# Performance work log

Hardware: AMD Instinct MI355X
Metric: run time of the kernel (lower is better)

The kernel has to match this reference:

```python
import jax, jax.numpy as jnp
import numpy as np

B, L, D, H, T = 64, 512, 768, 384, 9  # batch, seq_len, hidden, hidden//2, num_tags


def setup_inputs() -> dict:
    key = jax.random.key(0)
    ks = jax.random.split(key, 8)
    return {
        "encoder_out": jax.random.normal(ks[0], (B, L, D), jnp.float32),
        "ner_labels": jax.random.randint(ks[1], (B, L), 0, T),
        "mask": jnp.ones((B, L), jnp.bool_),
        "W1": jax.random.normal(ks[2], (D, H), jnp.float32) / np.sqrt(D).astype(np.float32),
        "b1": jnp.zeros((H,), jnp.float32),
        "W2": jax.random.normal(ks[3], (H, T), jnp.float32) / np.sqrt(H).astype(np.float32),
        "b2": jnp.zeros((T,), jnp.float32),
        "start_trans": jax.random.uniform(ks[4], (T,), jnp.float32, -0.1, 0.1),
        "end_trans": jax.random.uniform(ks[5], (T,), jnp.float32, -0.1, 0.1),
        "trans": jax.random.uniform(ks[6], (T, T), jnp.float32, -0.1, 0.1),
    }


def _crf_nll(emissions, tags, mask, start_trans, end_trans, trans):
    """-mean log-likelihood, matching pytorch-crf forward (reduction='mean')."""
    maskf = mask.astype(emissions.dtype)
    # ---- numerator: score of the gold tag path ----
    emit = jnp.take_along_axis(emissions, tags[..., None], axis=-1)[..., 0]  # [B,L]
    emit_score = jnp.sum(emit * maskf, axis=1)
    tr = trans[tags[:, :-1], tags[:, 1:]]  # [B,L-1]
    tr_score = jnp.sum(tr * maskf[:, 1:], axis=1)
    last_idx = jnp.sum(mask.astype(jnp.int32), axis=1) - 1
    last_tags = jnp.take_along_axis(tags, last_idx[:, None], axis=1)[:, 0]
    numer = start_trans[tags[:, 0]] + emit_score + tr_score + end_trans[last_tags]
    # ---- denominator: forward algorithm (log partition) via scan ----
    alpha0 = start_trans[None, :] + emissions[:, 0]          # [B,T]
    em_rest = jnp.swapaxes(emissions[:, 1:], 0, 1)           # [L-1,B,T]
    mk_rest = jnp.swapaxes(maskf[:, 1:], 0, 1)               # [L-1,B]

    def step(alpha, xs):
        e_t, m_t = xs
        nxt = jax.nn.logsumexp(alpha[:, :, None] + trans[None, :, :] + e_t[:, None, :], axis=1)
        return jnp.where(m_t[:, None] > 0, nxt, alpha), None

    alpha, _ = jax.lax.scan(step, alpha0, (em_rest, mk_rest))
    denom = jax.nn.logsumexp(alpha + end_trans[None, :], axis=1)
    return -jnp.mean(numer - denom)


def reference(encoder_out, ner_labels, mask, W1, b1, W2, b2, start_trans, end_trans, trans):
    # proj: Linear -> GELU (exact erf, torch default) -> Dropout (identity in eval)
    h = jax.nn.gelu(encoder_out @ W1 + b1, approximate=False)
    emissions = h @ W2 + b2  # [B,L,T]
    return _crf_nll(emissions, ner_labels, mask, start_trans, end_trans, trans)
```

## Files before the change

### kernel.cpp

```cpp
#include <hip/hip_runtime.h>
#include <hip/hip_bf16.h>
#include <math.h>

#define B_ 64
#define L_ 512
#define D_ 768
#define H_ 384
#define T_ 9
#define M_ (B_ * L_)

typedef __attribute__((ext_vector_type(8))) short short8;
typedef __attribute__((ext_vector_type(4))) float f32x4;

__device__ __forceinline__ unsigned short f2bf(float f) {
    unsigned u = __float_as_uint(f);
    u += 0x7FFFu + ((u >> 16) & 1u);
    return (unsigned short)(u >> 16);
}

__device__ __forceinline__ unsigned pkbf2(float a, float b) {
    __hip_bfloat162 h = __float22bfloat162_rn(float2{a, b});
    return *(unsigned*)&h;
}

__device__ __forceinline__ float gelu_fast(float x) {
    float z2 = 1.5957691216f * x + 0.0713548162726f * x * x * x;
    return x / (1.f + __expf(-z2));
}

__device__ __forceinline__ float wredf(float v) {
#pragma unroll
    for (int m = 32; m >= 1; m >>= 1) v += __shfl_xor(v, m, 64);
    return v;
}

__device__ __forceinline__ void sync_lds() {
    asm volatile("s_waitcnt lgkmcnt(0)\n\ts_barrier" ::: "memory");
}

__global__ __launch_bounds__(256) void prep_kernel(
    const float* __restrict__ W1, const float* __restrict__ W2,
    unsigned short* __restrict__ W1F, unsigned short* __restrict__ W2F,
    float* __restrict__ out)
{
    if (blockIdx.x == 0 && threadIdx.x == 0) out[0] = 0.f;
    const int g    = blockIdx.x * 4 + (threadIdx.x >> 6);
    const int lane = threadIdx.x & 63;
    const int lm   = lane & 15;
    const int q    = lane >> 4;
    if (g < 576) {
        const int nt = g / 24;
        const int kc = g - nt * 24;
        const int n  = nt * 16 + lm;
        short8 v;
#pragma unroll
        for (int j = 0; j < 8; ++j)
            v[j] = (short)f2bf(W1[(size_t)(kc * 32 + q * 8 + j) * H_ + n]);
        *(short8*)(W1F + ((size_t)g * 64 + lane) * 8) = v;
    } else if (g < 588) {
        const int kk = g - 576;
        short8 v;
#pragma unroll
        for (int j = 0; j < 8; ++j) {
            int k = kk * 32 + q * 8 + j;
            v[j] = (lm < 9) ? (short)f2bf(W2[(size_t)k * T_ + lm]) : (short)0;
        }
        *(short8*)(W2F + ((size_t)kk * 64 + lane) * 8) = v;
    }
}

__global__ __launch_bounds__(256) void emis_mfma_kernel(
    const float* __restrict__ X,
    const unsigned short* __restrict__ W1F,
    const float* __restrict__ b1,
    const unsigned short* __restrict__ W2F,
    const float* __restrict__ b2,
    float* __restrict__ em0,
    float* __restrict__ em1)
{
    __shared__ unsigned short Hs[64 * 200];
    unsigned short* As = Hs;

    const int t    = threadIdx.x;
    const int lane = t & 63;
    const int w    = t >> 6;
    const int lm   = lane & 15;
    const int q    = lane >> 4;
    const int half = blockIdx.x >> 9;
    const int rb   = blockIdx.x & 511;
    const int row0 = rb * 64;

    const int ar  = t >> 2;
    const int ako = (t & 3) << 3;
    const float* xp = X + (size_t)(row0 + ar) * D_ + ako;

    f32x4 acc[4][3];
#pragma unroll
    for (int mt = 0; mt < 4; ++mt)
#pragma unroll
        for (int i = 0; i < 3; ++i) acc[mt][i] = (f32x4)0.f;

    const int ntg0 = half * 12 + w * 3;

    {
        float4 p0 = *(const float4*)(xp);
        float4 p1 = *(const float4*)(xp + 4);
        int4 v = {(int)pkbf2(p0.x, p0.y), (int)pkbf2(p0.z, p0.w),
                  (int)pkbf2(p1.x, p1.y), (int)pkbf2(p1.z, p1.w)};
        *(int4*)&As[ar * 40 + ako] = v;
    }
    float4 xv[2][2];
    xv[0][0] = *(const float4*)(xp + 32);  xv[0][1] = *(const float4*)(xp + 36);
    xv[1][0] = *(const float4*)(xp + 64);  xv[1][1] = *(const float4*)(xp + 68);
    short8 bb[2][3];
#pragma unroll
    for (int i = 0; i < 3; ++i) {
        bb[0][i] = *(const short8*)(W1F + (((size_t)(ntg0 + i) * 24 + 0) * 64 + lane) * 8);
        bb[1][i] = *(const short8*)(W1F + (((size_t)(ntg0 + i) * 24 + 1) * 64 + lane) * 8);
    }

#pragma unroll
    for (int kc = 0; kc < 24; ++kc) {
        const int s = kc & 1;
        sync_lds();
        short8 af[4];
#pragma unroll
        for (int mt = 0; mt < 4; ++mt)
            af[mt] = *(const short8*)&As[s * 2560 + (mt * 16 + lm) * 40 + (q << 3)];
#pragma unroll
        for (int mt = 0; mt < 4; ++mt)
#pragma unroll
            for (int i = 0; i < 3; ++i)
                acc[mt][i] = __builtin_amdgcn_mfma_f32_16x16x32_bf16(
                    af[mt], bb[s][i], acc[mt][i], 0, 0, 0);
        if (kc < 23) {
            float4 x0 = xv[s][0], x1 = xv[s][1];
            int4 v = {(int)pkbf2(x0.x, x0.y), (int)pkbf2(x0.z, x0.w),
                      (int)pkbf2(x1.x, x1.y), (int)pkbf2(x1.z, x1.w)};
            *(int4*)&As[(s ^ 1) * 2560 + ar * 40 + ako] = v;
            if (kc < 21) {
                xv[s][0] = *(const float4*)(xp + (kc + 3) * 32);
                xv[s][1] = *(const float4*)(xp + (kc + 3) * 32 + 4);
            }
            if (kc < 22) {
#pragma unroll
                for (int i = 0; i < 3; ++i)
                    bb[s][i] = *(const short8*)(W1F +
                        (((size_t)(ntg0 + i) * 24 + kc + 2) * 64 + lane) * 8);
            }
        }
    }
    __syncthreads();

#pragma unroll
    for (int i = 0; i < 3; ++i) {
        const int lc = w * 48 + i * 16 + lm;
        const float b1v = b1[half * 192 + lc];
#pragma unroll
        for (int mt = 0; mt < 4; ++mt)
#pragma unroll
            for (int r = 0; r < 4; ++r) {
                float h = gelu_fast(acc[mt][i][r] + b1v);
                Hs[(mt * 16 + q * 4 + r) * 200 + lc] = f2bf(h);
            }
    }
    __syncthreads();

    f32x4 e = (f32x4)0.f;
#pragma unroll
    for (int kk = 0; kk < 6; ++kk) {
        short8 ah = *(const short8*)&Hs[(w * 16 + lm) * 200 + kk * 32 + (q << 3)];
        short8 bw = *(const short8*)(W2F + ((size_t)((half * 6 + kk) * 64 + lane)) * 8);
        e = __builtin_amdgcn_mfma_f32_16x16x32_bf16(ah, bw, e, 0, 0, 0);
    }
    if (lm < 9) {
        float* emo = half ? em1 : em0;
        const float badd = half ? 0.f : b2[lm];
#pragma unroll
        for (int r = 0; r < 4; ++r)
            emo[(size_t)(row0 + w * 16 + q * 4 + r) * T_ + lm] = e[r] + badd;
    }
}

__global__ __launch_bounds__(640) void crf_kernel(
    const float* __restrict__ em0,
    const float* __restrict__ em1,
    const int* __restrict__ labels,
    const unsigned char* __restrict__ maskb,
    const float* __restrict__ st,
    const float* __restrict__ et,
    const float* __restrict__ tr,
    float* __restrict__ out)
{
    const int b = blockIdx.x;
    const int t = threadIdx.x;

    __shared__ float es[64 * 73];
    __shared__ float Msa[64 * 81];
    __shared__ float Msb[32 * 81];
    __shared__ float trs[81];
    __shared__ float red_num;
    __shared__ unsigned char msh[L_];
    __shared__ int lbs[L_];

    const int mstride =
        (maskb[0] != 0 && maskb[1] == 0 && maskb[2] == 0 && maskb[3] == 0) ? 4 : 1;

    const float* e0 = em0 + (size_t)b * L_ * T_;
    const float* e1 = em1 + (size_t)b * L_ * T_;
    for (int i = t; i < L_ * T_; i += 640) {
        int tt = i / T_, j = i - tt * T_;
        es[(tt >> 3) * 73 + (tt & 7) * 9 + j] = e0[i] + e1[i];
    }
    if (t < 81) trs[t] = tr[t];
    for (int i = t; i < L_; i += 640) {
        msh[i] = maskb[((size_t)b * L_ + i) * (size_t)mstride];
        lbs[i] = labels[b * L_ + i];
    }
    __syncthreads();

    if (t < 576) {
        const int c  = t / 9;
        const int i0 = t - c * 9;
        float trr[81];
#pragma unroll
        for (int i = 0; i < 81; ++i) trr[i] = trs[i];
        float V[9];
#pragma unroll
        for (int j = 0; j < 9; ++j) V[j] = (j == i0) ? 0.f : -1e30f;

        const int sbeg = (c == 0) ? 1 : 0;
        for (int s = sbeg; s < 8; ++s) {
            int tt = c * 8 + s;
            if (msh[tt]) {
                const float* ep = &es[c * 73 + s * 9];
                float nv[9];
#pragma unroll
                for (int j = 0; j < 9; ++j) {
                    float a[9];
#pragma unroll
                    for (int k = 0; k < 9; ++k) a[k] = V[k] + trr[k * 9 + j];
                    float mx = a[0];
#pragma unroll
                    for (int k = 1; k < 9; ++k) mx = fmaxf(mx, a[k]);
                    float sum = 0.f;
#pragma unroll
                    for (int k = 0; k < 9; ++k) sum += __expf(a[k] - mx);
                    nv[j] = ep[j] + mx + __logf(sum);
                }
#pragma unroll
                for (int j = 0; j < 9; ++j) V[j] = nv[j];
            }
        }
#pragma unroll
        for (int j = 0; j < 9; ++j) Msa[c * 81 + i0 * 9 + j] = V[j];
    } else {
        const int lane = t - 576;
        float emit_s = 0.f, tr_sc = 0.f, mcnt = 0.f;
        for (int tt = lane; tt < L_; tt += 64) {
            if (msh[tt]) {
                mcnt += 1.f;
                int tag = lbs[tt];
                emit_s += es[(tt >> 3) * 73 + (tt & 7) * 9 + tag];
                if (tt >= 1) tr_sc += trs[lbs[tt - 1] * 9 + tag];
            }
        }
        emit_s = wredf(emit_s);
        tr_sc  = wredf(tr_sc);
        mcnt   = wredf(mcnt);
        if (lane == 0) {
            int last = (int)mcnt - 1;
            red_num = st[lbs[0]] + emit_s + tr_sc + et[lbs[last]];
        }
    }
    __syncthreads();

    float* src = Msa;
    float* dst = Msb;
    for (int n = 32; n >= 1; n >>= 1) {
        for (int idx = t; idx < n * 81; idx += 640) {
            int p = idx / 81;
            int r = idx - p * 81;
            int i = r / 9, j = r - i * 9;
            const float* A  = src + (2 * p) * 81 + i * 9;
            const float* Bm = src + (2 * p + 1) * 81 + j;
            float v[9];
#pragma unroll
            for (int k = 0; k < 9; ++k) v[k] = A[k] + Bm[k * 9];
            float mx = v[0];
#pragma unroll
            for (int k = 1; k < 9; ++k) mx = fmaxf(mx, v[k]);
            float sum = 0.f;
#pragma unroll
            for (int k = 0; k < 9; ++k) sum += __expf(v[k] - mx);
            dst[p * 81 + r] = mx + __logf(sum);
        }
        __syncthreads();
        float* tmp = src; src = dst; dst = tmp;
    }

    if (t < 64) {
        float v = -3.0e38f;
        if (t < 9) {
            float a[9];
#pragma unroll
            for (int i = 0; i < 9; ++i) a[i] = st[i] + es[i] + src[i * 9 + t];
            float mx = a[0];
#pragma unroll
            for (int i = 1; i < 9; ++i) mx = fmaxf(mx, a[i]);
            float sum = 0.f;
#pragma unroll
            for (int i = 0; i < 9; ++i) sum += __expf(a[i] - mx);
            v = mx + __logf(sum) + et[t];
        }
        float mx = v;
#pragma unroll
        for (int m = 32; m >= 1; m >>= 1) mx = fmaxf(mx, __shfl_xor(mx, m, 64));
        float sm = __expf(v - mx);
        sm = wredf(sm);
        if (t == 0) {
            float denom = mx + __logf(sm);
            atomicAdd(out, (denom - red_num) * (1.0f / (float)B_));
        }
    }
}

extern "C" void kernel_launch(void* const* d_in, const int* in_sizes, int n_in,
                              void* d_out, int out_size, void* d_ws, size_t ws_size,
                              hipStream_t stream) {
    const float*         enc    = (const float*)d_in[0];
    const int*           labels = (const int*)d_in[1];
    const unsigned char* mask   = (const unsigned char*)d_in[2];
    const float*         W1     = (const float*)d_in[3];
    const float*         b1     = (const float*)d_in[4];
    const float*         W2     = (const float*)d_in[5];
    const float*         b2     = (const float*)d_in[6];
    const float*         st     = (const float*)d_in[7];
    const float*         et     = (const float*)d_in[8];
    const float*         tr     = (const float*)d_in[9];

    float* em0          = (float*)d_ws;
    float* em1          = em0 + (size_t)M_ * T_;
    unsigned short* W1F = (unsigned short*)(em1 + (size_t)M_ * T_);
    unsigned short* W2F = W1F + (size_t)576 * 64 * 8;

    prep_kernel<<<147, 256, 0, stream>>>(W1, W2, W1F, W2F, (float*)d_out);
    emis_mfma_kernel<<<1024, 256, 0, stream>>>(enc, W1F, b1, W2F, b2, em0, em1);
    crf_kernel<<<B_, 640, 0, stream>>>(em0, em1, labels, mask, st, et, tr, (float*)d_out);
}
```

Before: 228.7 us.

## Stage X tiles via global_load_lds with swizzle and halve the row tile

The emission GEMM now copies fp32 X tiles straight into LDS with global_load_lds, using an XOR-swizzled layout, and converts them to bf16 after reading from LDS. Previously X went through registers and was converted before the LDS store. The row tile shrinks from 64 to 32, so the grid doubles to 2048 blocks, LDS per block drops, and launch bounds now request 5 waves' occupancy. The intent is better latency hiding and less register and VALU pressure. The cost is less reuse of each W1 fragment, a full vmcnt(0) wait plus barrier every K step, and half the waves sitting idle in the second GEMM.

New measurement: 242.1 us. +5.9%, slower.

```diff
diff --git a/kernel.cpp b/kernel.cpp
--- a/kernel.cpp
+++ b/kernel.cpp
@@ -34,8 +34,16 @@
     return v;
 }
 
-__device__ __forceinline__ void sync_lds() {
-    asm volatile("s_waitcnt lgkmcnt(0)\n\ts_barrier" ::: "memory");
+__device__ __forceinline__ short8 pack8(f32x4 a, f32x4 b) {
+    int4 v = {(int)pkbf2(a[0], a[1]), (int)pkbf2(a[2], a[3]),
+              (int)pkbf2(b[0], b[1]), (int)pkbf2(b[2], b[3])};
+    return *(short8*)&v;
+}
+
+__device__ __forceinline__ void stage16(const float* g, void* l) {
+    __builtin_amdgcn_global_load_lds(
+        (const __attribute__((address_space(1))) void*)g,
+        (__attribute__((address_space(3))) void*)l, 16, 0, 0);
 }
 
 __global__ __launch_bounds__(256) void prep_kernel(
@@ -69,7 +77,7 @@
     }
 }
 
-__global__ __launch_bounds__(256) void emis_mfma_kernel(
+__global__ __launch_bounds__(256, 5) void emis_mfma_kernel(
     const float* __restrict__ X,
     const unsigned short* __restrict__ W1F,
     const float* __restrict__ b1,
@@ -78,76 +86,75 @@
     float* __restrict__ em0,
     float* __restrict__ em1)
 {
-    __shared__ unsigned short Hs[64 * 200];
-    unsigned short* As = Hs;
+    __shared__ __align__(16) unsigned short Hs[32 * 200];
+    float* AsF = (float*)Hs;
 
     const int t    = threadIdx.x;
     const int lane = t & 63;
     const int w    = t >> 6;
     const int lm   = lane & 15;
     const int q    = lane >> 4;
-    const int half = blockIdx.x >> 9;
-    const int rb   = blockIdx.x & 511;
-    const int row0 = rb * 64;
-
-    const int ar  = t >> 2;
-    const int ako = (t & 3) << 3;
-    const float* xp = X + (size_t)(row0 + ar) * D_ + ako;
-
-    f32x4 acc[4][3];
-#pragma unroll
-    for (int mt = 0; mt < 4; ++mt)
+    const int half = blockIdx.x >> 10;
+    const int rb   = blockIdx.x & 1023;
+    const int row0 = rb * 32;
+
+    const int sr = t >> 3;
+    const int sc = (t & 7) ^ (sr & 7);
+    const float* sp = X + (size_t)(row0 + sr) * D_ + sc * 4;
+    char* l0 = (char*)Hs + w * 1024;
+    char* l1 = l0 + 4096;
+
+    const int ntg0 = half * 12 + w * 3;
+
+    const int e7  = lm & 7;
+    const int co0 = (((q * 2 + 0) ^ e7) << 2);
+    const int co1 = (((q * 2 + 1) ^ e7) << 2);
+
+    f32x4 acc[2][3];
+#pragma unroll
+    for (int mt = 0; mt < 2; ++mt)
 #pragma unroll
         for (int i = 0; i < 3; ++i) acc[mt][i] = (f32x4)0.f;
 
-    const int ntg0 = half * 12 + w * 3;
-
-    {
-        float4 p0 = *(const float4*)(xp);
-        float4 p1 = *(const float4*)(xp + 4);
-        int4 v = {(int)pkbf2(p0.x, p0.y), (int)pkbf2(p0.z, p0.w),
-                  (int)pkbf2(p1.x, p1.y), (int)pkbf2(p1.z, p1.w)};
-        *(int4*)&As[ar * 40 + ako] = v;
-    }
-    float4 xv[2][2];
-    xv[0][0] = *(const float4*)(xp + 32);  xv[0][1] = *(const float4*)(xp + 36);
-    xv[1][0] = *(const float4*)(xp + 64);  xv[1][1] = *(const float4*)(xp + 68);
-    short8 bb[2][3];
-#pragma unroll
-    for (int i = 0; i < 3; ++i) {
-        bb[0][i] = *(const short8*)(W1F + (((size_t)(ntg0 + i) * 24 + 0) * 64 + lane) * 8);
-        bb[1][i] = *(const short8*)(W1F + (((size_t)(ntg0 + i) * 24 + 1) * 64 + lane) * 8);
-    }
+    stage16(sp, l0);
+    short8 bb[3];
+#pragma unroll
+    for (int i = 0; i < 3; ++i)
+        bb[i] = *(const short8*)(W1F + (((size_t)(ntg0 + i) * 24 + 0) * 64 + lane) * 8);
+    asm volatile("s_waitcnt vmcnt(0)" ::: "memory");
+    __builtin_amdgcn_s_barrier();
 
 #pragma unroll
     for (int kc = 0; kc < 24; ++kc) {
         const int s = kc & 1;
-        sync_lds();
-        short8 af[4];
-#pragma unroll
-        for (int mt = 0; mt < 4; ++mt)
-            af[mt] = *(const short8*)&As[s * 2560 + (mt * 16 + lm) * 40 + (q << 3)];
-#pragma unroll
-        for (int mt = 0; mt < 4; ++mt)
+        if (kc < 23) stage16(sp + (kc + 1) * 32, s ? l0 : l1);
+        short8 bbn[3];
+        if (kc < 23) {
+#pragma unroll
+            for (int i = 0; i < 3; ++i)
+                bbn[i] = *(const short8*)(W1F +
+                    (((size_t)(ntg0 + i) * 24 + kc + 1) * 64 + lane) * 8);
+        }
+        const float* fb = AsF + s * 1024;
+        short8 af[2];
+#pragma unroll
+        for (int mt = 0; mt < 2; ++mt) {
+            const float* rp = fb + (mt * 16 + lm) * 32;
+            f32x4 a0 = *(const f32x4*)(rp + co0);
+            f32x4 a1 = *(const f32x4*)(rp + co1);
+            af[mt] = pack8(a0, a1);
+        }
+#pragma unroll
+        for (int mt = 0; mt < 2; ++mt)
 #pragma unroll
             for (int i = 0; i < 3; ++i)
                 acc[mt][i] = __builtin_amdgcn_mfma_f32_16x16x32_bf16(
-                    af[mt], bb[s][i], acc[mt][i], 0, 0, 0);
+                    af[mt], bb[i], acc[mt][i], 0, 0, 0);
         if (kc < 23) {
-            float4 x0 = xv[s][0], x1 = xv[s][1];
-            int4 v = {(int)pkbf2(x0.x, x0.y), (int)pkbf2(x0.z, x0.w),
-                      (int)pkbf2(x1.x, x1.y), (int)pkbf2(x1.z, x1.w)};
-            *(int4*)&As[(s ^ 1) * 2560 + ar * 40 + ako] = v;
-            if (kc < 21) {
-                xv[s][0] = *(const float4*)(xp + (kc + 3) * 32);
-                xv[s][1] = *(const float4*)(xp + (kc + 3) * 32 + 4);
-            }
-            if (kc < 22) {
-#pragma unroll
-                for (int i = 0; i < 3; ++i)
-                    bb[s][i] = *(const short8*)(W1F +
-                        (((size_t)(ntg0 + i) * 24 + kc + 2) * 64 + lane) * 8);
-            }
+#pragma unroll
+            for (int i = 0; i < 3; ++i) bb[i] = bbn[i];
+            asm volatile("s_waitcnt vmcnt(0)" ::: "memory");
+            __builtin_amdgcn_s_barrier();
         }
     }
     __syncthreads();
@@ -157,7 +164,7 @@
         const int lc = w * 48 + i * 16 + lm;
         const float b1v = b1[half * 192 + lc];
 #pragma unroll
-        for (int mt = 0; mt < 4; ++mt)
+        for (int mt = 0; mt < 2; ++mt)
 #pragma unroll
             for (int r = 0; r < 4; ++r) {
                 float h = gelu_fast(acc[mt][i][r] + b1v);
@@ -166,19 +173,21 @@
     }
     __syncthreads();
 
-    f32x4 e = (f32x4)0.f;
-#pragma unroll
-    for (int kk = 0; kk < 6; ++kk) {
-        short8 ah = *(const short8*)&Hs[(w * 16 + lm) * 200 + kk * 32 + (q << 3)];
-        short8 bw = *(const short8*)(W2F + ((size_t)((half * 6 + kk) * 64 + lane)) * 8);
-        e = __builtin_amdgcn_mfma_f32_16x16x32_bf16(ah, bw, e, 0, 0, 0);
-    }
-    if (lm < 9) {
-        float* emo = half ? em1 : em0;
-        const float badd = half ? 0.f : b2[lm];
-#pragma unroll
-        for (int r = 0; r < 4; ++r)
-            emo[(size_t)(row0 + w * 16 + q * 4 + r) * T_ + lm] = e[r] + badd;
+    if (w < 2) {
+        f32x4 e = (f32x4)0.f;
+#pragma unroll
+        for (int kk = 0; kk < 6; ++kk) {
+            short8 ah = *(const short8*)&Hs[(w * 16 + lm) * 200 + kk * 32 + (q << 3)];
+            short8 bw = *(const short8*)(W2F + ((size_t)((half * 6 + kk) * 64 + lane)) * 8);
+            e = __builtin_amdgcn_mfma_f32_16x16x32_bf16(ah, bw, e, 0, 0, 0);
+        }
+        if (lm < 9) {
+            float* emo = half ? em1 : em0;
+            const float badd = half ? 0.f : b2[lm];
+#pragma unroll
+            for (int r = 0; r < 4; ++r)
+                emo[(size_t)(row0 + w * 16 + q * 4 + r) * T_ + lm] = e[r] + badd;
+        }
     }
 }
 
@@ -345,6 +354,6 @@
     unsigned short* W2F = W1F + (size_t)576 * 64 * 8;
 
     prep_kernel<<<147, 256, 0, stream>>>(W1, W2, W1F, W2F, (float*)d_out);
-    emis_mfma_kernel<<<1024, 256, 0, stream>>>(enc, W1F, b1, W2F, b2, em0, em1);
+    emis_mfma_kernel<<<2048, 256, 0, stream>>>(enc, W1F, b1, W2F, b2, em0, em1);
     crf_kernel<<<B_, 640, 0, stream>>>(em0, em1, labels, mask, st, et, tr, (float*)d_out);
 }
```

## Load X fragments directly from global into MFMA operands, dropping LDS staging

Applied to the files above, without the earlier changes.

Replaces the LDS double-buffered staging of the X tile with direct per-wave global loads that are packed to bf16 straight into MFMA A-fragments. This removes the per-iteration barriers and LDS traffic. The cost is that each of the 4 waves now re-reads the full 64-row X tile from global/L2, which is 4x the global read traffic, and the manual prefetch pipelining is gone. Launch bounds now request 3 blocks per CU to raise occupancy and hide the added latency.

After: 292.1 us. 27.7% more time.

```diff
diff --git a/kernel.cpp b/kernel.cpp
--- a/kernel.cpp
+++ b/kernel.cpp
@@ -34,8 +34,10 @@
     return v;
 }
 
-__device__ __forceinline__ void sync_lds() {
-    asm volatile("s_waitcnt lgkmcnt(0)\n\ts_barrier" ::: "memory");
+__device__ __forceinline__ short8 pack8(f32x4 a, f32x4 b) {
+    int4 v = {(int)pkbf2(a[0], a[1]), (int)pkbf2(a[2], a[3]),
+              (int)pkbf2(b[0], b[1]), (int)pkbf2(b[2], b[3])};
+    return *(short8*)&v;
 }
 
 __global__ __launch_bounds__(256) void prep_kernel(
@@ -69,7 +71,7 @@
     }
 }
 
-__global__ __launch_bounds__(256) void emis_mfma_kernel(
+__global__ __launch_bounds__(256, 3) void emis_mfma_kernel(
     const float* __restrict__ X,
     const unsigned short* __restrict__ W1F,
     const float* __restrict__ b1,
@@ -78,8 +80,7 @@
     float* __restrict__ em0,
     float* __restrict__ em1)
 {
-    __shared__ unsigned short Hs[64 * 200];
-    unsigned short* As = Hs;
+    __shared__ __align__(16) unsigned short Hs[64 * 200];
 
     const int t    = threadIdx.x;
     const int lane = t & 63;
@@ -90,9 +91,16 @@
     const int rb   = blockIdx.x & 511;
     const int row0 = rb * 64;
 
-    const int ar  = t >> 2;
-    const int ako = (t & 3) << 3;
-    const float* xp = X + (size_t)(row0 + ar) * D_ + ako;
+    const int ntg0 = half * 12 + w * 3;
+
+    const float* xr0 = X + (size_t)(row0 +  0 + lm) * D_ + (q << 3);
+    const float* xr1 = xr0 + (size_t)16 * D_;
+    const float* xr2 = xr0 + (size_t)32 * D_;
+    const float* xr3 = xr0 + (size_t)48 * D_;
+
+    const unsigned short* wp0 = W1F + ((size_t)(ntg0 + 0) * 24 * 64 + lane) * 8;
+    const unsigned short* wp1 = W1F + ((size_t)(ntg0 + 1) * 24 * 64 + lane) * 8;
+    const unsigned short* wp2 = W1F + ((size_t)(ntg0 + 2) * 24 * 64 + lane) * 8;
 
     f32x4 acc[4][3];
 #pragma unroll
@@ -100,57 +108,33 @@
 #pragma unroll
         for (int i = 0; i < 3; ++i) acc[mt][i] = (f32x4)0.f;
 
-    const int ntg0 = half * 12 + w * 3;
-
-    {
-        float4 p0 = *(const float4*)(xp);
-        float4 p1 = *(const float4*)(xp + 4);
-        int4 v = {(int)pkbf2(p0.x, p0.y), (int)pkbf2(p0.z, p0.w),
-                  (int)pkbf2(p1.x, p1.y), (int)pkbf2(p1.z, p1.w)};
-        *(int4*)&As[ar * 40 + ako] = v;
-    }
-    float4 xv[2][2];
-    xv[0][0] = *(const float4*)(xp + 32);  xv[0][1] = *(const float4*)(xp + 36);
-    xv[1][0] = *(const float4*)(xp + 64);  xv[1][1] = *(const float4*)(xp + 68);
-    short8 bb[2][3];
-#pragma unroll
-    for (int i = 0; i < 3; ++i) {
-        bb[0][i] = *(const short8*)(W1F + (((size_t)(ntg0 + i) * 24 + 0) * 64 + lane) * 8);
-        bb[1][i] = *(const short8*)(W1F + (((size_t)(ntg0 + i) * 24 + 1) * 64 + lane) * 8);
-    }
-
 #pragma unroll
     for (int kc = 0; kc < 24; ++kc) {
-        const int s = kc & 1;
-        sync_lds();
-        short8 af[4];
-#pragma unroll
-        for (int mt = 0; mt < 4; ++mt)
-            af[mt] = *(const short8*)&As[s * 2560 + (mt * 16 + lm) * 40 + (q << 3)];
-#pragma unroll
-        for (int mt = 0; mt < 4; ++mt)
-#pragma unroll
-            for (int i = 0; i < 3; ++i)
-                acc[mt][i] = __builtin_amdgcn_mfma_f32_16x16x32_bf16(
-                    af[mt], bb[s][i], acc[mt][i], 0, 0, 0);
-        if (kc < 23) {
-            float4 x0 = xv[s][0], x1 = xv[s][1];
-            int4 v = {(int)pkbf2(x0.x, x0.y), (int)pkbf2(x0.z, x0.w),
-                      (int)pkbf2(x1.x, x1.y), (int)pkbf2(x1.z, x1.w)};
-            *(int4*)&As[(s ^ 1) * 2560 + ar * 40 + ako] = v;
-            if (kc < 21) {
-                xv[s][0] = *(const float4*)(xp + (kc + 3) * 32);
-                xv[s][1] = *(const float4*)(xp + (kc + 3) * 32 + 4);
-            }
-            if (kc < 22) {
-#pragma unroll
-                for (int i = 0; i < 3; ++i)
-                    bb[s][i] = *(const short8*)(W1F +
-                        (((size_t)(ntg0 + i) * 24 + kc + 2) * 64 + lane) * 8);
-            }
-        }
-    }
-    __syncthreads();
+        short8 af0 = pack8(*(const f32x4*)(xr0 + kc * 32),
+                           *(const f32x4*)(xr0 + kc * 32 + 4));
+        short8 af1 = pack8(*(const f32x4*)(xr1 + kc * 32),
+                           *(const f32x4*)(xr1 + kc * 32 + 4));
+        short8 af2 = pack8(*(const f32x4*)(xr2 + kc * 32),
+                           *(const f32x4*)(xr2 + kc * 32 + 4));
+        short8 af3 = pack8(*(const f32x4*)(xr3 + kc * 32),
+                           *(const f32x4*)(xr3 + kc * 32 + 4));
+        short8 bw0 = *(const short8*)(wp0 + (size_t)kc * 512);
+        short8 bw1 = *(const short8*)(wp1 + (size_t)kc * 512);
+        short8 bw2 = *(const short8*)(wp2 + (size_t)kc * 512);
+
+        acc[0][0] = __builtin_amdgcn_mfma_f32_16x16x32_bf16(af0, bw0, acc[0][0], 0, 0, 0);
+        acc[0][1] = __builtin_amdgcn_mfma_f32_16x16x32_bf16(af0, bw1, acc[0][1], 0, 0, 0);
+        acc[0][2] = __builtin_amdgcn_mfma_f32_16x16x32_bf16(af0, bw2, acc[0][2], 0, 0, 0);
+        acc[1][0] = __builtin_amdgcn_mfma_f32_16x16x32_bf16(af1, bw0, acc[1][0], 0, 0, 0);
+        acc[1][1] = __builtin_amdgcn_mfma_f32_16x16x32_bf16(af1, bw1, acc[1][1], 0, 0, 0);
+        acc[1][2] = __builtin_amdgcn_mfma_f32_16x16x32_bf16(af1, bw2, acc[1][2], 0, 0, 0);
+        acc[2][0] = __builtin_amdgcn_mfma_f32_16x16x32_bf16(af2, bw0, acc[2][0], 0, 0, 0);
+        acc[2][1] = __builtin_amdgcn_mfma_f32_16x16x32_bf16(af2, bw1, acc[2][1], 0, 0, 0);
+        acc[2][2] = __builtin_amdgcn_mfma_f32_16x16x32_bf16(af2, bw2, acc[2][2], 0, 0, 0);
+        acc[3][0] = __builtin_amdgcn_mfma_f32_16x16x32_bf16(af3, bw0, acc[3][0], 0, 0, 0);
+        acc[3][1] = __builtin_amdgcn_mfma_f32_16x16x32_bf16(af3, bw1, acc[3][1], 0, 0, 0);
+        acc[3][2] = __builtin_amdgcn_mfma_f32_16x16x32_bf16(af3, bw2, acc[3][2], 0, 0, 0);
+    }
 
 #pragma unroll
     for (int i = 0; i < 3; ++i) {
```
